# Kernel optimization log

Measured on AMD Instinct MI355X. Metric: run time of the kernel, lower is better.

Reference implementation:

```python
import jax, jax.numpy as jnp
import numpy as np

B, S, D, F, E = 4, 1024, 768, 3072, 8


def setup_inputs() -> dict:
    key = jax.random.key(0)
    k0, k1, k2, k3 = jax.random.split(key, 4)
    hidden_states = jax.random.normal(k0, (B, S, D), dtype=jnp.float32)
    w_router = jax.random.normal(k1, (D, E), dtype=jnp.float32) * 0.02
    w1 = jax.random.normal(k2, (E, D, F), dtype=jnp.float32) * 0.02
    b1 = jnp.zeros((E, F), dtype=jnp.float32)
    w2 = jax.random.normal(k3, (E, F, D), dtype=jnp.float32) * 0.02
    b2 = jnp.zeros((E, D), dtype=jnp.float32)
    return {"hidden_states": hidden_states, "w_router": w_router,
            "w1": w1, "b1": b1, "w2": w2, "b2": b2}


def reference(hidden_states, w_router, w1, b1, w2, b2):
    # Switch-style top-1 router: logits -> softmax -> one-hot mask + max prob
    router_logits = jnp.einsum("bsd,de->bse", hidden_states, w_router)
    router_probs_full = jax.nn.softmax(router_logits, axis=-1)
    expert_index = jnp.argmax(router_probs_full, axis=-1)            # [B,S] int
    router_probs = jnp.max(router_probs_full, axis=-1, keepdims=True)  # [B,S,1]
    router_mask = jax.nn.one_hot(expert_index, E, dtype=hidden_states.dtype)  # [B,S,E]

    # Dispatch/compute/combine: each token goes to exactly one expert FFN.
    # Loop over the small fixed expert set (E=8), combine via the one-hot mask;
    # math is identical to the gather -> expert FFN -> scatter of the original.
    out = jnp.zeros_like(hidden_states)
    for e in range(E):
        h = jax.nn.relu(jnp.einsum("bsd,df->bsf", hidden_states, w1[e]) + b1[e])
        h = jnp.einsum("bsf,fd->bsd", h, w2[e]) + b2[e]
        out = out + router_mask[..., e:e + 1] * h

    hidden_out = router_probs * out  # scale by top-1 router prob, as in original
    return hidden_out, router_logits, expert_index
```

## Files before the change

### kernel.cpp

```cpp
#include <hip/hip_runtime.h>
#include <hip/hip_bf16.h>

#define T_TOK 4096
#define DIM   768
#define FF    3072
#define NE    8

typedef __attribute__((ext_vector_type(8))) short bf16x8;
typedef __attribute__((ext_vector_type(4))) short bf16x4;
typedef __attribute__((ext_vector_type(4))) float f32x4;
typedef __attribute__((ext_vector_type(2))) float f32x2;

__device__ __forceinline__ unsigned short f2bf(float f) {
    union { float f; unsigned int u; } v; v.f = f;
    unsigned int u = v.u;
    u += 0x7FFFu + ((u >> 16) & 1u);
    return (unsigned short)(u >> 16);
}

__device__ __forceinline__ bf16x8 pack8(f32x4 a, f32x4 b) {
    bf16x8 r;
    r[0] = (short)f2bf(a[0]); r[1] = (short)f2bf(a[1]);
    r[2] = (short)f2bf(a[2]); r[3] = (short)f2bf(a[3]);
    r[4] = (short)f2bf(b[0]); r[5] = (short)f2bf(b[1]);
    r[6] = (short)f2bf(b[2]); r[7] = (short)f2bf(b[3]);
    return r;
}

__global__ __launch_bounds__(256) void k_router(
    const float* __restrict__ x, const float* __restrict__ wr,
    float* __restrict__ out_logits, float* __restrict__ out_eidx,
    float* __restrict__ probs, int* __restrict__ counts, int* __restrict__ bucket)
{
    int tok  = (blockIdx.x * 256 + threadIdx.x) >> 6;
    int lane = threadIdx.x & 63;
    if (tok >= T_TOK) return;
    const float* xr = x + (size_t)tok * DIM;
    float acc[NE];
    #pragma unroll
    for (int e = 0; e < NE; e++) acc[e] = 0.f;
    #pragma unroll
    for (int j = 0; j < DIM / 64; j++) {
        int d = j * 64 + lane;
        float xv = xr[d];
        const float* wrow = wr + (size_t)d * NE;
        #pragma unroll
        for (int e = 0; e < NE; e++) acc[e] += xv * wrow[e];
    }
    #pragma unroll
    for (int e = 0; e < NE; e++) {
        #pragma unroll
        for (int off = 32; off >= 1; off >>= 1)
            acc[e] += __shfl_xor(acc[e], off);
    }
    if (lane == 0) {
        float mx = acc[0]; int mi = 0;
        #pragma unroll
        for (int e = 1; e < NE; e++) if (acc[e] > mx) { mx = acc[e]; mi = e; }
        float se = 0.f;
        #pragma unroll
        for (int e = 0; e < NE; e++) se += __expf(acc[e] - mx);
        #pragma unroll
        for (int e = 0; e < NE; e++) out_logits[(size_t)tok * NE + e] = acc[e];
        out_eidx[tok] = (float)mi;
        probs[tok] = 1.f / se;
        int pos = atomicAdd(&counts[mi], 1);
        bucket[mi * T_TOK + pos] = tok;
    }
}

__global__ void k_compact(const int* __restrict__ counts, int* __restrict__ offsets,
                          const int* __restrict__ bucket, int* __restrict__ sorted)
{
    __shared__ int soff[NE + 1];
    if (threadIdx.x == 0) {
        int s = 0;
        for (int e = 0; e < NE; e++) { soff[e] = s; s += counts[e]; }
        soff[NE] = s;
        for (int e = 0; e <= NE; e++) offsets[e] = soff[e];
    }
    __syncthreads();
    for (int e = 0; e < NE; e++) {
        int c = counts[e], o = soff[e];
        for (int i = threadIdx.x; i < c; i += blockDim.x)
            sorted[o + i] = bucket[e * T_TOK + i];
    }
}

__global__ __launch_bounds__(256) void k_gather(
    const float* __restrict__ x, const int* __restrict__ sorted,
    unsigned short* __restrict__ Xg)
{
    int g0 = (blockIdx.x * 256 + threadIdx.x) * 8;
    if (g0 >= T_TOK * DIM) return;
    int row = g0 / DIM, col = g0 - row * DIM;
    const float* src = x + (size_t)sorted[row] * DIM + col;
    f32x4 a = *(const f32x4*)(src);
    f32x4 b = *(const f32x4*)(src + 4);
    *(bf16x8*)(Xg + (size_t)row * DIM + col) = pack8(a, b);
}

__global__ __launch_bounds__(256, 3) void k_gemm1(
    const unsigned short* __restrict__ Xg, const float* __restrict__ w1,
    const float* __restrict__ b1, const int* __restrict__ counts,
    const int* __restrict__ offsets, unsigned short* __restrict__ Hbuf)
{
    const int e   = blockIdx.y >> 5;
    const int ti  = blockIdx.y & 31;
    const int cnt = counts[e];
    if (ti * 128 >= cnt) return;
    const int n0    = blockIdx.x * 128;
    const int off   = offsets[e];
    const int rbase = ti * 128;
    const int rmax  = cnt - rbase - 1;
    const int tid   = threadIdx.x;
    const int lane  = tid & 63;
    const int wave  = tid >> 6;
    const int wm = wave >> 1, wn = wave & 1;

    __shared__ unsigned short As[128][72];
    __shared__ unsigned short Bs[128][72];

    const float* w1e = w1 + (size_t)e * DIM * FF;
    f32x4 acc[4][4];
    #pragma unroll
    for (int i = 0; i < 4; i++)
        #pragma unroll
        for (int j = 0; j < 4; j++) acc[i][j] = (f32x4)0.f;

    const int arow = tid >> 1, aseg = tid & 1;
    const int are  = (arow <= rmax) ? arow : 0;
    const unsigned short* abase = Xg + (size_t)(off + rbase + are) * DIM + aseg * 32;
    const int kb = tid >> 5, nb = tid & 31;
    const float* bbase = w1e + (size_t)kb * 8 * FF + n0 + nb * 4;

    bf16x8 aR[4];
    f32x4  bR[8];
    #pragma unroll
    for (int j = 0; j < 4; j++) aR[j] = *(const bf16x8*)(abase + j * 8);
    #pragma unroll
    for (int r = 0; r < 8; r++) bR[r] = *(const f32x4*)(bbase + (size_t)r * FF);

    const int lrow = lane & 15, kq = lane >> 4;

    for (int it = 0; it < DIM / 64; ++it) {
        __syncthreads();
        #pragma unroll
        for (int j = 0; j < 4; j++)
            *(bf16x8*)&As[arow][aseg * 32 + j * 8] = aR[j];
        #pragma unroll
        for (int j = 0; j < 4; j++) {
            bf16x8 c;
            #pragma unroll
            for (int r = 0; r < 8; r++) c[r] = (short)f2bf(bR[r][j]);
            *(bf16x8*)&Bs[nb * 4 + j][kb * 8] = c;
        }
        __syncthreads();
        if (it + 1 < DIM / 64) {
            const unsigned short* an = abase + (it + 1) * 64;
            #pragma unroll
            for (int j = 0; j < 4; j++) aR[j] = *(const bf16x8*)(an + j * 8);
            const float* bn = bbase + (size_t)(it + 1) * 64 * FF;
            #pragma unroll
            for (int r = 0; r < 8; r++) bR[r] = *(const f32x4*)(bn + (size_t)r * FF);
        }
        #pragma unroll
        for (int ks = 0; ks < 2; ks++) {
            bf16x8 af[4], bfr[4];
            #pragma unroll
            for (int i = 0; i < 4; i++)
                af[i] = *(const bf16x8*)&As[wm * 64 + i * 16 + lrow][ks * 32 + kq * 8];
            #pragma unroll
            for (int i = 0; i < 4; i++)
                bfr[i] = *(const bf16x8*)&Bs[wn * 64 + i * 16 + lrow][ks * 32 + kq * 8];
            #pragma unroll
            for (int mi = 0; mi < 4; mi++)
                #pragma unroll
                for (int ni = 0; ni < 4; ni++)
                    acc[mi][ni] = __builtin_amdgcn_mfma_f32_16x16x32_bf16(
                        af[mi], bfr[ni], acc[mi][ni], 0, 0, 0);
        }
    }

    const int quad = lane >> 4;
    #pragma unroll
    for (int ni = 0; ni < 4; ni++) {
        int gn = n0 + wn * 64 + ni * 16 + lrow;
        float bias = b1[e * FF + gn];
        #pragma unroll
        for (int mi = 0; mi < 4; mi++) {
            f32x4 v = acc[mi][ni];
            #pragma unroll
            for (int r = 0; r < 4; r++) {
                int ml = wm * 64 + mi * 16 + quad * 4 + r;
                if (rbase + ml < cnt) {
                    float h = v[r] + bias;
                    h = h > 0.f ? h : 0.f;
                    Hbuf[(size_t)(off + rbase + ml) * FF + gn] = f2bf(h);
                }
            }
        }
    }
}

__global__ __launch_bounds__(256, 4) void k_gemm2(
    const unsigned short* __restrict__ Hbuf, const float* __restrict__ w2,
    const float* __restrict__ b2, const int* __restrict__ sorted,
    const int* __restrict__ counts, const int* __restrict__ offsets,
    const float* __restrict__ probs, float* __restrict__ outh)
{
    const int e   = blockIdx.y >> 5;
    const int ti  = blockIdx.y & 31;
    const int cnt = counts[e];
    if (ti * 128 >= cnt) return;
    const int n0    = blockIdx.x * 64;
    const int off   = offsets[e];
    const int rbase = ti * 128;
    const int rmax  = cnt - rbase - 1;
    const int tid   = threadIdx.x;
    const int lane  = tid & 63;
    const int wave  = tid >> 6;
    const int wm = wave >> 1, wn = wave & 1;

    __shared__ unsigned short As[128][72];
    __shared__ unsigned short Bs[64][72];
    __shared__ int   s_tok[128];
    __shared__ float s_prob[128];

    if (tid < 128) {
        int r = rbase + tid;
        int tk = sorted[off + ((r < cnt) ? r : rbase)];
        s_tok[tid]  = tk;
        s_prob[tid] = probs[tk];
    }

    const float* w2e = w2 + (size_t)e * FF * DIM;
    f32x4 acc[4][2];
    #pragma unroll
    for (int i = 0; i < 4; i++)
        #pragma unroll
        for (int j = 0; j < 2; j++) acc[i][j] = (f32x4)0.f;

    const int arow = tid >> 1, aseg = tid & 1;
    const int are  = (arow <= rmax) ? arow : 0;
    const unsigned short* abase = Hbuf + (size_t)(off + rbase + are) * FF + aseg * 32;
    const int kb = tid >> 5, nb = tid & 31;
    const float* bbase = w2e + (size_t)kb * 8 * DIM + n0 + nb * 2;

    bf16x8 aR[4];
    f32x2  bR[8];
    #pragma unroll
    for (int j = 0; j < 4; j++) aR[j] = *(const bf16x8*)(abase + j * 8);
    #pragma unroll
    for (int r = 0; r < 8; r++) bR[r] = *(const f32x2*)(bbase + (size_t)r * DIM);

    const int lrow = lane & 15, kq = lane >> 4;

    for (int it = 0; it < FF / 64; ++it) {
        __syncthreads();
        #pragma unroll
        for (int j = 0; j < 4; j++)
            *(bf16x8*)&As[arow][aseg * 32 + j * 8] = aR[j];
        {
            bf16x8 c0, c1;
            #pragma unroll
            for (int r = 0; r < 8; r++) { c0[r] = (short)f2bf(bR[r][0]); c1[r] = (short)f2bf(bR[r][1]); }
            *(bf16x8*)&Bs[nb * 2 + 0][kb * 8] = c0;
            *(bf16x8*)&Bs[nb * 2 + 1][kb * 8] = c1;
        }
        __syncthreads();
        if (it + 1 < FF / 64) {
            const unsigned short* an = abase + (it + 1) * 64;
            #pragma unroll
            for (int j = 0; j < 4; j++) aR[j] = *(const bf16x8*)(an + j * 8);
            const float* bn = bbase + (size_t)(it + 1) * 64 * DIM;
            #pragma unroll
            for (int r = 0; r < 8; r++) bR[r] = *(const f32x2*)(bn + (size_t)r * DIM);
        }
        #pragma unroll
        for (int ks = 0; ks < 2; ks++) {
            bf16x8 af[4], bfr[2];
            #pragma unroll
            for (int i = 0; i < 4; i++)
                af[i] = *(const bf16x8*)&As[wm * 64 + i * 16 + lrow][ks * 32 + kq * 8];
            #pragma unroll
            for (int i = 0; i < 2; i++)
                bfr[i] = *(const bf16x8*)&Bs[wn * 32 + i * 16 + lrow][ks * 32 + kq * 8];
            #pragma unroll
            for (int mi = 0; mi < 4; mi++)
                #pragma unroll
                for (int ni = 0; ni < 2; ni++)
                    acc[mi][ni] = __builtin_amdgcn_mfma_f32_16x16x32_bf16(
                        af[mi], bfr[ni], acc[mi][ni], 0, 0, 0);
        }
    }

    const int quad = lane >> 4;
    #pragma unroll
    for (int ni = 0; ni < 2; ni++) {
        int gn = n0 + wn * 32 + ni * 16 + lrow;
        float bias = b2[e * DIM + gn];
        #pragma unroll
        for (int mi = 0; mi < 4; mi++) {
            f32x4 v = acc[mi][ni];
            #pragma unroll
            for (int r = 0; r < 4; r++) {
                int ml = wm * 64 + mi * 16 + quad * 4 + r;
                if (rbase + ml < cnt) {
                    outh[(size_t)s_tok[ml] * DIM + gn] = (v[r] + bias) * s_prob[ml];
                }
            }
        }
    }
}

extern "C" void kernel_launch(void* const* d_in, const int* in_sizes, int n_in,
                              void* d_out, int out_size, void* d_ws, size_t ws_size,
                              hipStream_t stream) {
    (void)in_sizes; (void)n_in; (void)out_size; (void)ws_size;
    const float* x  = (const float*)d_in[0];
    const float* wr = (const float*)d_in[1];
    const float* w1 = (const float*)d_in[2];
    const float* b1 = (const float*)d_in[3];
    const float* w2 = (const float*)d_in[4];
    const float* b2 = (const float*)d_in[5];

    float* out_hidden = (float*)d_out;
    float* out_logits = out_hidden + (size_t)T_TOK * DIM;
    float* out_eidx   = out_logits + (size_t)T_TOK * NE;

    char* ws = (char*)d_ws;
    int*   counts  = (int*)(ws + 0);
    int*   offsets = (int*)(ws + 64);
    float* probs   = (float*)(ws + 128);
    int*   sorted  = (int*)(ws + 16512);
    int*   bucket  = (int*)(ws + 32896);
    unsigned short* Xg   = (unsigned short*)(ws + 163968);
    unsigned short* Hbuf = (unsigned short*)(ws + 6455424);

    hipMemsetAsync(counts, 0, 32, stream);
    k_router<<<dim3(T_TOK / 4), dim3(256), 0, stream>>>(
        x, wr, out_logits, out_eidx, probs, counts, bucket);
    k_compact<<<dim3(1), dim3(256), 0, stream>>>(counts, offsets, bucket, sorted);
    k_gather<<<dim3((T_TOK * DIM / 8 + 255) / 256), dim3(256), 0, stream>>>(x, sorted, Xg);
    k_gemm1<<<dim3(FF / 128, NE * 32), dim3(256), 0, stream>>>(
        Xg, w1, b1, counts, offsets, Hbuf);
    k_gemm2<<<dim3(DIM / 64, NE * 32), dim3(256), 0, stream>>>(
        Hbuf, w2, b2, sorted, counts, offsets, probs, out_hidden);
}
```

Before: 413.0 us.

## Pre-transpose weights to bf16 and use direct global-to-LDS loads with split-K atomics

Adds kernels that convert x to bf16 and transpose/convert both expert weight tensors to bf16 K-major layout each call. The GEMMs then load tiles straight into LDS with global_load_lds, use gathered token rows instead of a packed copy, and split the second GEMM's K across four blocks that atomically accumulate into an output pre-initialised with bias times prob. This removes the per-tile fp32-to-bf16 conversion and register staging inside the GEMM loops. In exchange it adds full weight conversion traffic every call, float atomics in the output, and a large workspace, with the old path kept as a fallback when the workspace is too small.

```diff
diff --git a/kernel.cpp b/kernel.cpp
--- a/kernel.cpp
+++ b/kernel.cpp
@@ -10,6 +10,13 @@
 typedef __attribute__((ext_vector_type(4))) short bf16x4;
 typedef __attribute__((ext_vector_type(4))) float f32x4;
 typedef __attribute__((ext_vector_type(2))) float f32x2;
+
+typedef __attribute__((address_space(1))) void gvoid_t;
+typedef __attribute__((address_space(3))) void lvoid_t;
+
+__device__ __forceinline__ void g2l16(const void* g, void* l) {
+    __builtin_amdgcn_global_load_lds((gvoid_t*)(void*)g, (lvoid_t*)l, 16, 0, 0);
+}
 
 __device__ __forceinline__ unsigned short f2bf(float f) {
     union { float f; unsigned int u; } v; v.f = f;
@@ -30,7 +37,8 @@
 __global__ __launch_bounds__(256) void k_router(
     const float* __restrict__ x, const float* __restrict__ wr,
     float* __restrict__ out_logits, float* __restrict__ out_eidx,
-    float* __restrict__ probs, int* __restrict__ counts, int* __restrict__ bucket)
+    float* __restrict__ probs, int* __restrict__ eidx_i,
+    int* __restrict__ counts, int* __restrict__ bucket)
 {
     int tok  = (blockIdx.x * 256 + threadIdx.x) >> 6;
     int lane = threadIdx.x & 63;
@@ -63,6 +71,7 @@
         #pragma unroll
         for (int e = 0; e < NE; e++) out_logits[(size_t)tok * NE + e] = acc[e];
         out_eidx[tok] = (float)mi;
+        eidx_i[tok] = mi;
         probs[tok] = 1.f / se;
         int pos = atomicAdd(&counts[mi], 1);
         bucket[mi * T_TOK + pos] = tok;
@@ -87,7 +96,234 @@
     }
 }
 
-__global__ __launch_bounds__(256) void k_gather(
+__global__ __launch_bounds__(256) void k_xconv(
+    const float* __restrict__ x, unsigned short* __restrict__ Xb)
+{
+    int g0 = (blockIdx.x * 256 + threadIdx.x) * 8;
+    if (g0 >= T_TOK * DIM) return;
+    f32x4 a = *(const f32x4*)(x + g0);
+    f32x4 b = *(const f32x4*)(x + g0 + 4);
+    *(bf16x8*)(Xb + g0) = pack8(a, b);
+}
+
+__global__ __launch_bounds__(256) void k_tconv(
+    const float* __restrict__ in, unsigned short* __restrict__ out, int R, int C)
+{
+    const size_t es = (size_t)R * C;
+    in  += blockIdx.z * es;
+    out += blockIdx.z * es;
+    const int c0 = blockIdx.x * 64, r0 = blockIdx.y * 64;
+    __shared__ unsigned short t[64][72];
+    const int tr = threadIdx.x >> 2, tc = (threadIdx.x & 3) * 16;
+    const float* src = in + (size_t)(r0 + tr) * C + c0 + tc;
+    f32x4 v0 = *(const f32x4*)(src);
+    f32x4 v1 = *(const f32x4*)(src + 4);
+    f32x4 v2 = *(const f32x4*)(src + 8);
+    f32x4 v3 = *(const f32x4*)(src + 12);
+    #pragma unroll
+    for (int j = 0; j < 4; j++) {
+        t[tc + j][tr]      = f2bf(v0[j]);
+        t[tc + 4 + j][tr]  = f2bf(v1[j]);
+        t[tc + 8 + j][tr]  = f2bf(v2[j]);
+        t[tc + 12 + j][tr] = f2bf(v3[j]);
+    }
+    __syncthreads();
+    const int oc = threadIdx.x >> 2, orr = (threadIdx.x & 3) * 16;
+    bf16x8 o0, o1;
+    #pragma unroll
+    for (int j = 0; j < 8; j++) { o0[j] = t[oc][orr + j]; o1[j] = t[oc][orr + 8 + j]; }
+    unsigned short* dst = out + (size_t)(c0 + oc) * R + r0 + orr;
+    *(bf16x8*)(dst)     = o0;
+    *(bf16x8*)(dst + 8) = o1;
+}
+
+__global__ __launch_bounds__(256) void k_init(
+    const float* __restrict__ b2, const int* __restrict__ eidx,
+    const float* __restrict__ probs, float* __restrict__ outh)
+{
+    int tok = blockIdx.x;
+    int e = eidx[tok];
+    float p = probs[tok];
+    const float* br = b2 + e * DIM;
+    for (int d = threadIdx.x; d < DIM; d += 256)
+        outh[(size_t)tok * DIM + d] = br[d] * p;
+}
+
+__global__ __launch_bounds__(256, 3) void k_gemm1(
+    const unsigned short* __restrict__ Xb, const unsigned short* __restrict__ wt1,
+    const float* __restrict__ b1, const int* __restrict__ sorted,
+    const int* __restrict__ counts, const int* __restrict__ offsets,
+    unsigned short* __restrict__ Hbuf)
+{
+    const int e  = blockIdx.y >> 5;
+    const int ti = blockIdx.y & 31;
+    const int cnt = counts[e];
+    if (ti * 128 >= cnt) return;
+    const int n0 = blockIdx.x * 128;
+    const int off = offsets[e];
+    const int rbase = ti * 128;
+    const int tid = threadIdx.x, lane = tid & 63, wave = tid >> 6;
+    const int wm = wave >> 1, wn = wave & 1;
+
+    __shared__ unsigned short As[128][32];
+    __shared__ unsigned short Bs[128][32];
+
+    const int lr = lane >> 2;
+    const int ls = (lane & 3) * 8;
+
+    int r0 = rbase + wave * 32 + lr;        if (r0 >= cnt) r0 = rbase;
+    int r1 = rbase + wave * 32 + 16 + lr;   if (r1 >= cnt) r1 = rbase;
+    const unsigned short* aP0 = Xb + (size_t)sorted[off + r0] * DIM + ls;
+    const unsigned short* aP1 = Xb + (size_t)sorted[off + r1] * DIM + ls;
+    const unsigned short* wB  = wt1 + (size_t)e * FF * DIM;
+    const unsigned short* bP0 = wB + (size_t)(n0 + wave * 32 + lr) * DIM + ls;
+    const unsigned short* bP1 = wB + (size_t)(n0 + wave * 32 + 16 + lr) * DIM + ls;
+    unsigned short* lA0 = &As[wave * 32][0];
+    unsigned short* lA1 = &As[wave * 32 + 16][0];
+    unsigned short* lB0 = &Bs[wave * 32][0];
+    unsigned short* lB1 = &Bs[wave * 32 + 16][0];
+
+    f32x4 acc[4][4];
+    #pragma unroll
+    for (int i = 0; i < 4; i++)
+        #pragma unroll
+        for (int j = 0; j < 4; j++) acc[i][j] = (f32x4)0.f;
+
+    const int lrow = lane & 15, kq = lane >> 4;
+
+    for (int k0 = 0; k0 < DIM; k0 += 32) {
+        __syncthreads();
+        g2l16(aP0 + k0, lA0);
+        g2l16(aP1 + k0, lA1);
+        g2l16(bP0 + k0, lB0);
+        g2l16(bP1 + k0, lB1);
+        __syncthreads();
+        bf16x8 af[4], bfv[4];
+        #pragma unroll
+        for (int i = 0; i < 4; i++)
+            af[i] = *(const bf16x8*)&As[wm * 64 + i * 16 + lrow][kq * 8];
+        #pragma unroll
+        for (int i = 0; i < 4; i++)
+            bfv[i] = *(const bf16x8*)&Bs[wn * 64 + i * 16 + lrow][kq * 8];
+        #pragma unroll
+        for (int mi = 0; mi < 4; mi++)
+            #pragma unroll
+            for (int ni = 0; ni < 4; ni++)
+                acc[mi][ni] = __builtin_amdgcn_mfma_f32_16x16x32_bf16(
+                    af[mi], bfv[ni], acc[mi][ni], 0, 0, 0);
+    }
+
+    const int quad = lane >> 4;
+    #pragma unroll
+    for (int ni = 0; ni < 4; ni++) {
+        int gn = n0 + wn * 64 + ni * 16 + lrow;
+        float bias = b1[e * FF + gn];
+        #pragma unroll
+        for (int mi = 0; mi < 4; mi++) {
+            f32x4 v = acc[mi][ni];
+            #pragma unroll
+            for (int r = 0; r < 4; r++) {
+                int ml = rbase + wm * 64 + mi * 16 + quad * 4 + r;
+                if (ml < cnt) {
+                    float h = v[r] + bias; h = h > 0.f ? h : 0.f;
+                    Hbuf[(size_t)(off + ml) * FF + gn] = f2bf(h);
+                }
+            }
+        }
+    }
+}
+
+__global__ __launch_bounds__(256, 3) void k_gemm2(
+    const unsigned short* __restrict__ Hbuf, const unsigned short* __restrict__ wt2,
+    const int* __restrict__ sorted, const int* __restrict__ counts,
+    const int* __restrict__ offsets, const float* __restrict__ probs,
+    float* __restrict__ outh)
+{
+    const int e  = blockIdx.y >> 5;
+    const int ti = blockIdx.y & 31;
+    const int cnt = counts[e];
+    if (ti * 128 >= cnt) return;
+    const int n0 = blockIdx.x * 128;
+    const int kc = blockIdx.z;
+    const int off = offsets[e];
+    const int rbase = ti * 128;
+    const int tid = threadIdx.x, lane = tid & 63, wave = tid >> 6;
+    const int wm = wave >> 1, wn = wave & 1;
+
+    __shared__ unsigned short As[128][32];
+    __shared__ unsigned short Bs[128][32];
+    __shared__ int   s_tok[128];
+    __shared__ float s_prob[128];
+
+    if (tid < 128) {
+        int rr = rbase + tid; if (rr >= cnt) rr = rbase;
+        int tk = sorted[off + rr];
+        s_tok[tid]  = tk;
+        s_prob[tid] = probs[tk];
+    }
+
+    const int lr = lane >> 2, ls = (lane & 3) * 8;
+    int r0 = rbase + wave * 32 + lr;        if (r0 >= cnt) r0 = rbase;
+    int r1 = rbase + wave * 32 + 16 + lr;   if (r1 >= cnt) r1 = rbase;
+    const unsigned short* aP0 = Hbuf + (size_t)(off + r0) * FF + kc * 768 + ls;
+    const unsigned short* aP1 = Hbuf + (size_t)(off + r1) * FF + kc * 768 + ls;
+    const unsigned short* wB  = wt2 + (size_t)e * DIM * FF;
+    const unsigned short* bP0 = wB + (size_t)(n0 + wave * 32 + lr) * FF + kc * 768 + ls;
+    const unsigned short* bP1 = wB + (size_t)(n0 + wave * 32 + 16 + lr) * FF + kc * 768 + ls;
+    unsigned short* lA0 = &As[wave * 32][0];
+    unsigned short* lA1 = &As[wave * 32 + 16][0];
+    unsigned short* lB0 = &Bs[wave * 32][0];
+    unsigned short* lB1 = &Bs[wave * 32 + 16][0];
+
+    f32x4 acc[4][4];
+    #pragma unroll
+    for (int i = 0; i < 4; i++)
+        #pragma unroll
+        for (int j = 0; j < 4; j++) acc[i][j] = (f32x4)0.f;
+
+    const int lrow = lane & 15, kq = lane >> 4;
+
+    for (int k0 = 0; k0 < 768; k0 += 32) {
+        __syncthreads();
+        g2l16(aP0 + k0, lA0);
+        g2l16(aP1 + k0, lA1);
+        g2l16(bP0 + k0, lB0);
+        g2l16(bP1 + k0, lB1);
+        __syncthreads();
+        bf16x8 af[4], bfv[4];
+        #pragma unroll
+        for (int i = 0; i < 4; i++)
+            af[i] = *(const bf16x8*)&As[wm * 64 + i * 16 + lrow][kq * 8];
+        #pragma unroll
+        for (int i = 0; i < 4; i++)
+            bfv[i] = *(const bf16x8*)&Bs[wn * 64 + i * 16 + lrow][kq * 8];
+        #pragma unroll
+        for (int mi = 0; mi < 4; mi++)
+            #pragma unroll
+            for (int ni = 0; ni < 4; ni++)
+                acc[mi][ni] = __builtin_amdgcn_mfma_f32_16x16x32_bf16(
+                    af[mi], bfv[ni], acc[mi][ni], 0, 0, 0);
+    }
+
+    const int quad = lane >> 4;
+    #pragma unroll
+    for (int ni = 0; ni < 4; ni++) {
+        int gn = n0 + wn * 64 + ni * 16 + lrow;
+        #pragma unroll
+        for (int mi = 0; mi < 4; mi++) {
+            f32x4 v = acc[mi][ni];
+            #pragma unroll
+            for (int r = 0; r < 4; r++) {
+                int mloc = wm * 64 + mi * 16 + quad * 4 + r;
+                if (rbase + mloc < cnt) {
+                    atomicAdd(&outh[(size_t)s_tok[mloc] * DIM + gn], v[r] * s_prob[mloc]);
+                }
+            }
+        }
+    }
+}
+
+__global__ __launch_bounds__(256) void k_gather_fb(
     const float* __restrict__ x, const int* __restrict__ sorted,
     unsigned short* __restrict__ Xg)
 {
@@ -100,7 +336,7 @@
     *(bf16x8*)(Xg + (size_t)row * DIM + col) = pack8(a, b);
 }
 
-__global__ __launch_bounds__(256, 3) void k_gemm1(
+__global__ __launch_bounds__(256, 3) void k_gemm1_fb(
     const unsigned short* __restrict__ Xg, const float* __restrict__ w1,
     const float* __restrict__ b1, const int* __restrict__ counts,
     const int* __restrict__ offsets, unsigned short* __restrict__ Hbuf)
@@ -117,32 +353,26 @@
     const int lane  = tid & 63;
     const int wave  = tid >> 6;
     const int wm = wave >> 1, wn = wave & 1;
-
     __shared__ unsigned short As[128][72];
     __shared__ unsigned short Bs[128][72];
-
     const float* w1e = w1 + (size_t)e * DIM * FF;
     f32x4 acc[4][4];
     #pragma unroll
     for (int i = 0; i < 4; i++)
         #pragma unroll
         for (int j = 0; j < 4; j++) acc[i][j] = (f32x4)0.f;
-
     const int arow = tid >> 1, aseg = tid & 1;
     const int are  = (arow <= rmax) ? arow : 0;
     const unsigned short* abase = Xg + (size_t)(off + rbase + are) * DIM + aseg * 32;
     const int kb = tid >> 5, nb = tid & 31;
     const float* bbase = w1e + (size_t)kb * 8 * FF + n0 + nb * 4;
-
     bf16x8 aR[4];
     f32x4  bR[8];
     #pragma unroll
     for (int j = 0; j < 4; j++) aR[j] = *(const bf16x8*)(abase + j * 8);
     #pragma unroll
     for (int r = 0; r < 8; r++) bR[r] = *(const f32x4*)(bbase + (size_t)r * FF);
-
     const int lrow = lane & 15, kq = lane >> 4;
-
     for (int it = 0; it < DIM / 64; ++it) {
         __syncthreads();
         #pragma unroll
@@ -181,7 +411,6 @@
                         af[mi], bfr[ni], acc[mi][ni], 0, 0, 0);
         }
     }
-
     const int quad = lane >> 4;
     #pragma unroll
     for (int ni = 0; ni < 4; ni++) {
@@ -203,7 +432,7 @@
     }
 }
 
-__global__ __launch_bounds__(256, 4) void k_gemm2(
+__global__ __launch_bounds__(256, 4) void k_gemm2_fb(
     const unsigned short* __restrict__ Hbuf, const float* __restrict__ w2,
     const float* __restrict__ b2, const int* __restrict__ sorted,
     const int* __restrict__ counts, const int* __restrict__ offsets,
@@ -221,41 +450,34 @@
     const int lane  = tid & 63;
     const int wave  = tid >> 6;
     const int wm = wave >> 1, wn = wave & 1;
-
     __shared__ unsigned short As[128][72];
     __shared__ unsigned short Bs[64][72];
     __shared__ int   s_tok[128];
     __shared__ float s_prob[128];
-
     if (tid < 128) {
         int r = rbase + tid;
         int tk = sorted[off + ((r < cnt) ? r : rbase)];
         s_tok[tid]  = tk;
         s_prob[tid] = probs[tk];
     }
-
     const float* w2e = w2 + (size_t)e * FF * DIM;
     f32x4 acc[4][2];
     #pragma unroll
     for (int i = 0; i < 4; i++)
         #pragma unroll
         for (int j = 0; j < 2; j++) acc[i][j] = (f32x4)0.f;
-
     const int arow = tid >> 1, aseg = tid & 1;
     const int are  = (arow <= rmax) ? arow : 0;
     const unsigned short* abase = Hbuf + (size_t)(off + rbase + are) * FF + aseg * 32;
     const int kb = tid >> 5, nb = tid & 31;
     const float* bbase = w2e + (size_t)kb * 8 * DIM + n0 + nb * 2;
-
     bf16x8 aR[4];
     f32x2  bR[8];
     #pragma unroll
     for (int j = 0; j < 4; j++) aR[j] = *(const bf16x8*)(abase + j * 8);
     #pragma unroll
     for (int r = 0; r < 8; r++) bR[r] = *(const f32x2*)(bbase + (size_t)r * DIM);
-
     const int lrow = lane & 15, kq = lane >> 4;
-
     for (int it = 0; it < FF / 64; ++it) {
         __syncthreads();
         #pragma unroll
@@ -294,7 +516,6 @@
                         af[mi], bfr[ni], acc[mi][ni], 0, 0, 0);
         }
     }
-
     const int quad = lane >> 4;
     #pragma unroll
     for (int ni = 0; ni < 2; ni++) {
@@ -317,7 +538,7 @@
 extern "C" void kernel_launch(void* const* d_in, const int* in_sizes, int n_in,
                               void* d_out, int out_size, void* d_ws, size_t ws_size,
                               hipStream_t stream) {
-    (void)in_sizes; (void)n_in; (void)out_size; (void)ws_size;
+    (void)in_sizes; (void)n_in; (void)out_size;
     const float* x  = (const float*)d_in[0];
     const float* wr = (const float*)d_in[1];
     const float* w1 = (const float*)d_in[2];
@@ -333,18 +554,34 @@
     int*   counts  = (int*)(ws + 0);
     int*   offsets = (int*)(ws + 64);
     float* probs   = (float*)(ws + 128);
-    int*   sorted  = (int*)(ws + 16512);
-    int*   bucket  = (int*)(ws + 32896);
-    unsigned short* Xg   = (unsigned short*)(ws + 163968);
-    unsigned short* Hbuf = (unsigned short*)(ws + 6455424);
+    int*   eidx_i  = (int*)(ws + 16512);
+    int*   sorted  = (int*)(ws + 32896);
+    int*   bucket  = (int*)(ws + 49280);
+    unsigned short* Xb   = (unsigned short*)(ws + 180352);
+    unsigned short* Hbuf = (unsigned short*)(ws + 6471808);
+    unsigned short* wt1  = (unsigned short*)(ws + 31637632);
+    unsigned short* wt2  = (unsigned short*)(ws + 69386368);
+    const size_t NEED = 107135104;
 
     hipMemsetAsync(counts, 0, 32, stream);
     k_router<<<dim3(T_TOK / 4), dim3(256), 0, stream>>>(
-        x, wr, out_logits, out_eidx, probs, counts, bucket);
+        x, wr, out_logits, out_eidx, probs, eidx_i, counts, bucket);
     k_compact<<<dim3(1), dim3(256), 0, stream>>>(counts, offsets, bucket, sorted);
-    k_gather<<<dim3((T_TOK * DIM / 8 + 255) / 256), dim3(256), 0, stream>>>(x, sorted, Xg);
-    k_gemm1<<<dim3(FF / 128, NE * 32), dim3(256), 0, stream>>>(
-        Xg, w1, b1, counts, offsets, Hbuf);
-    k_gemm2<<<dim3(DIM / 64, NE * 32), dim3(256), 0, stream>>>(
-        Hbuf, w2, b2, sorted, counts, offsets, probs, out_hidden);
-}
+
+    if (ws_size >= NEED) {
+        k_xconv<<<dim3(T_TOK * DIM / 8 / 256), dim3(256), 0, stream>>>(x, Xb);
+        k_tconv<<<dim3(FF / 64, DIM / 64, NE), dim3(256), 0, stream>>>(w1, wt1, DIM, FF);
+        k_tconv<<<dim3(DIM / 64, FF / 64, NE), dim3(256), 0, stream>>>(w2, wt2, FF, DIM);
+        k_init<<<dim3(T_TOK), dim3(256), 0, stream>>>(b2, eidx_i, probs, out_hidden);
+        k_gemm1<<<dim3(FF / 128, NE * 32), dim3(256), 0, stream>>>(
+            Xb, wt1, b1, sorted, counts, offsets, Hbuf);
+        k_gemm2<<<dim3(DIM / 128, NE * 32, 4), dim3(256), 0, stream>>>(
+            Hbuf, wt2, sorted, counts, offsets, probs, out_hidden);
+    } else {
+        k_gather_fb<<<dim3(T_TOK * DIM / 8 / 256), dim3(256), 0, stream>>>(x, sorted, Xb);
+        k_gemm1_fb<<<dim3(FF / 128, NE * 32), dim3(256), 0, stream>>>(
+            Xb, w1, b1, counts, offsets, Hbuf);
+        k_gemm2_fb<<<dim3(DIM / 64, NE * 32), dim3(256), 0, stream>>>(
+            Hbuf, w2, b2, sorted, counts, offsets, probs, out_hidden);
+    }
+}
```

Result: faster. 390.7 us (-5.4%).
